# Optimization experiments

Hardware: AMD Instinct MI355X
Metric: run time of the kernel (lower is better)

The kernel has to match this reference:

```python
import jax, jax.numpy as jnp
import numpy as np

N_NODES = 200000
N_EDGES = 600000
IN_DIM = 130   # hidden_dim + 2
HID = 128
BN_EPS = 1e-5


def setup_inputs() -> dict:
    key = jax.random.key(0)
    ks = jax.random.split(key, 12)
    s = 0.05
    inp = {
        'x': jax.random.normal(ks[0], (N_NODES, IN_DIM), dtype=jnp.float32),
        'edge_index': jax.random.randint(ks[1], (2, N_EDGES), 0, N_NODES, dtype=jnp.int32),
        # SAGEConv 1: lin_l (aggregated neighbors, with bias), lin_r (root, no bias)
        'W1_l': jax.random.normal(ks[2], (IN_DIM, HID), dtype=jnp.float32) * s,
        'b1_l': jnp.zeros((HID,), dtype=jnp.float32),
        'W1_r': jax.random.normal(ks[3], (IN_DIM, HID), dtype=jnp.float32) * s,
        # BatchNorm1d(128) params + running stats (eval mode)
        'g1': jnp.ones((HID,), dtype=jnp.float32),
        'be1': jnp.zeros((HID,), dtype=jnp.float32),
        'rm1': jax.random.normal(ks[4], (HID,), dtype=jnp.float32) * 0.01,
        'rv1': jnp.ones((HID,), dtype=jnp.float32),
        # SAGEConv 2
        'W2_l': jax.random.normal(ks[5], (HID, HID), dtype=jnp.float32) * s,
        'b2_l': jnp.zeros((HID,), dtype=jnp.float32),
        'W2_r': jax.random.normal(ks[6], (HID, HID), dtype=jnp.float32) * s,
        'g2': jnp.ones((HID,), dtype=jnp.float32),
        'be2': jnp.zeros((HID,), dtype=jnp.float32),
        'rm2': jax.random.normal(ks[7], (HID,), dtype=jnp.float32) * 0.01,
        'rv2': jnp.ones((HID,), dtype=jnp.float32),
    }
    return inp


def _sage_mean(x, src, dst, W_l, b_l, W_r, n_nodes):
    # PyG SAGEConv (mean aggr): out = lin_l(mean_{j in N(i)} x_j) + lin_r(x_i)
    msg = x[src]                                                 # [E, F] gather
    agg = jax.ops.segment_sum(msg, dst, num_segments=n_nodes)    # [N, F]
    deg = jax.ops.segment_sum(jnp.ones((src.shape[0], 1), x.dtype), dst,
                              num_segments=n_nodes)              # [N, 1]
    mean = agg / jnp.maximum(deg, 1.0)
    return mean @ W_l + b_l + x @ W_r


def _bn_eval(x, g, b, rm, rv):
    return (x - rm) * (g * jax.lax.rsqrt(rv + BN_EPS)) + b


def reference(x, edge_index, W1_l, b1_l, W1_r, g1, be1, rm1, rv1,
              W2_l, b2_l, W2_r, g2, be2, rm2, rv2):
    src, dst = edge_index[0], edge_index[1]
    n = x.shape[0]
    h = _sage_mean(x, src, dst, W1_l, b1_l, W1_r, n)
    h = jax.nn.relu(_bn_eval(h, g1, be1, rm1, rv1))
    # dropout is identity in eval mode
    h = _sage_mean(h, src, dst, W2_l, b2_l, W2_r, n)
    h = jax.nn.relu(_bn_eval(h, g2, be2, rm2, rv2))
    return h
```

## Files before the change

kernel.cpp:

```cpp
#include <hip/hip_runtime.h>

typedef short v8s __attribute__((ext_vector_type(8)));
typedef float v4f __attribute__((ext_vector_type(4)));
typedef unsigned short v4us __attribute__((ext_vector_type(4)));

__device__ __forceinline__ unsigned short f2bf(float x) {
  union { float f; unsigned int u; } c; c.f = x;
  unsigned int u = c.u;
  return (unsigned short)((u + 0x7fffu + ((u >> 16) & 1u)) >> 16);
}
__device__ __forceinline__ float bf2f(unsigned int hi16) {
  union { unsigned int u; float f; } c; c.u = hi16 << 16;
  return c.f;
}
__device__ __forceinline__ ushort2 pk(float2 v) {
  ushort2 p; p.x = f2bf(v.x); p.y = f2bf(v.y); return p;
}

__global__ void bn_fold_k(const float* __restrict__ g1, const float* __restrict__ be1,
                          const float* __restrict__ rm1, const float* __restrict__ rv1,
                          const float* __restrict__ b1,
                          const float* __restrict__ g2, const float* __restrict__ be2,
                          const float* __restrict__ rm2, const float* __restrict__ rv2,
                          const float* __restrict__ b2,
                          float* __restrict__ s1, float* __restrict__ t1,
                          float* __restrict__ s2, float* __restrict__ t2,
                          unsigned short* __restrict__ bufA, int N) {
  int i = threadIdx.x;
  if (i < 128) {
    float sv = g1[i] * rsqrtf(rv1[i] + 1e-5f);
    s1[i] = sv; t1[i] = (b1[i] - rm1[i]) * sv + be1[i];
    float sw = g2[i] * rsqrtf(rv2[i] + 1e-5f);
    s2[i] = sw; t2[i] = (b2[i] - rm2[i]) * sw + be2[i];
  }
  if (i < 64) ((unsigned int*)(bufA + (long)N * 128))[i] = 0u;
}

template<int K, int KC>
__global__ void pack2_k(const float* __restrict__ Wl, const float* __restrict__ Wr,
                        unsigned short* __restrict__ wpk) {
  int i = blockIdx.x * 256 + threadIdx.x;
  if (i >= KC * 8192) return;
  int kk = i & 31, n = (i >> 5) & 255, kc = i >> 13;
  int k = kc * 32 + kk;
  float v = 0.f;
  if (k < K) v = (n < 128) ? Wl[k * 128 + n] : Wr[k * 128 + (n - 128)];
  wpk[i] = f2bf(v);
}

__global__ void zero_i_k(int* __restrict__ p, int n) {
  int i = blockIdx.x * 256 + threadIdx.x;
  if (i < n) p[i] = 0;
}
__global__ void count_k(const int* __restrict__ dst, int* __restrict__ degi, int E) {
  int i = blockIdx.x * 256 + threadIdx.x;
  if (i < E) atomicAdd(&degi[dst[i]], 1);
}
__global__ __launch_bounds__(256) void scan1_k(const int* __restrict__ degi,
                                               int* __restrict__ rowptr,
                                               int* __restrict__ bsum, int N) {
  __shared__ int sd[256];
  const int t = threadIdx.x;
  const int base = blockIdx.x * 1024 + t * 4;
  int v[4];
#pragma unroll
  for (int j = 0; j < 4; ++j) v[j] = (base + j < N) ? degi[base + j] : 0;
  const int tot = v[0] + v[1] + v[2] + v[3];
  sd[t] = tot;
  __syncthreads();
  for (int off = 1; off < 256; off <<= 1) {
    int o = (t >= off) ? sd[t - off] : 0;
    __syncthreads();
    sd[t] += o;
    __syncthreads();
  }
  int e = sd[t] - tot;
#pragma unroll
  for (int j = 0; j < 4; ++j) {
    if (base + j < N) rowptr[base + j] = e;
    e += v[j];
  }
  if (t == 255) bsum[blockIdx.x] = sd[255];
}
__global__ __launch_bounds__(256) void scan2_k(int* __restrict__ bsum, int nb) {
  __shared__ int sd[256];
  const int t = threadIdx.x;
  const int v = (t < nb) ? bsum[t] : 0;
  sd[t] = v;
  __syncthreads();
  for (int off = 1; off < 256; off <<= 1) {
    int o = (t >= off) ? sd[t - off] : 0;
    __syncthreads();
    sd[t] += o;
    __syncthreads();
  }
  if (t < nb) bsum[t] = sd[t] - v;
}
__global__ void scan3_k(int* __restrict__ rowptr, int* __restrict__ cursor,
                        const int* __restrict__ bsum, int N, int E) {
  int i = blockIdx.x * 256 + threadIdx.x;
  if (i < N) {
    int v = rowptr[i] + bsum[i >> 10];
    rowptr[i] = v;
    cursor[i] = v;
  } else if (i == N) {
    rowptr[N] = E;
  }
}
__global__ void fill_k(const int* __restrict__ src, const int* __restrict__ dst,
                       int* __restrict__ cursor, int* __restrict__ nbr, int E) {
  int i = blockIdx.x * 256 + threadIdx.x;
  if (i < E) {
    int p = atomicAdd(&cursor[dst[i]], 1);
    nbr[p] = src[i];
  }
}

template<int KC, bool SRCF32>
__global__ __launch_bounds__(256) void gemm2_k(const void* __restrict__ Asrc,
                                               const unsigned short* __restrict__ wpk,
                                               unsigned short* __restrict__ Ol,
                                               unsigned short* __restrict__ Or, int N) {
  constexpr int KP = KC * 32;
  constexpr int LDA = KP + 8;
  __shared__ __align__(16) unsigned short a_s[64][LDA];
  const int tid = threadIdx.x;
  const int node0 = blockIdx.x * 64;

  if constexpr (SRCF32) {
    {
      const int zr = tid >> 2, zq = tid & 3;
      v8s z = {0, 0, 0, 0, 0, 0, 0, 0};
      *(v8s*)&a_s[zr][136 + zq * 8] = z;
      if (tid < 192) {
        const int r3 = tid / 3, p3 = tid - 3 * r3;
        *(unsigned int*)&a_s[r3][130 + 2 * p3] = 0u;
      }
    }
    const float* xb = (const float*)Asrc + (long)node0 * 130;
    if (node0 + 64 <= N) {
      float4 v[9];
#pragma unroll
      for (int i = 0; i < 9; ++i) {
        const int g = i * 256 + tid;
        if (g < 2080) v[i] = *(const float4*)(xb + 4 * g);
      }
#pragma unroll
      for (int i = 0; i < 9; ++i) {
        const int g = i * 256 + tid;
        if (g < 2080) {
          const int p0 = 2 * g, p1 = 2 * g + 1;
          const int r0_ = (p0 * 4033) >> 18, r1_ = (p1 * 4033) >> 18;
          const int c0_ = p0 - 65 * r0_, c1_ = p1 - 65 * r1_;
          *(ushort2*)&a_s[r0_][2 * c0_] = pk(make_float2(v[i].x, v[i].y));
          *(ushort2*)&a_s[r1_][2 * c1_] = pk(make_float2(v[i].z, v[i].w));
        }
      }
    } else {
      for (int i = 0; i < 9; ++i) {
        const int g = i * 256 + tid;
        if (g < 2080) {
#pragma unroll
          for (int h = 0; h < 2; ++h) {
            const int p = 2 * g + h;
            const int r = (p * 4033) >> 18;
            const int c = p - 65 * r;
            float2 vv = make_float2(0.f, 0.f);
            if (node0 + r < N)
              vv = *(const float2*)((const float*)Asrc + (long)(node0 + r) * 130 + 2 * c);
            *(ushort2*)&a_s[r][2 * c] = pk(vv);
          }
        }
      }
    }
  } else {
    const unsigned short* hb = (const unsigned short*)Asrc + (long)node0 * 128;
    v8s v[KC];
#pragma unroll
    for (int i = 0; i < KC; ++i) {
      const int u = i * 256 + tid;
      const int r = u >> 4;
      v[i] = (v8s){0, 0, 0, 0, 0, 0, 0, 0};
      if (node0 + r < N) v[i] = *(const v8s*)(hb + 8 * u);
    }
#pragma unroll
    for (int i = 0; i < KC; ++i) {
      const int u = i * 256 + tid;
      *(v8s*)&a_s[u >> 4][(u & 15) * 8] = v[i];
    }
  }
  __syncthreads();

  const int wave = tid >> 6, lane = tid & 63;
  const int quad = lane >> 4, l16 = lane & 15;
  v4f acc[4][4];
#pragma unroll
  for (int mt = 0; mt < 4; ++mt)
#pragma unroll
    for (int nt = 0; nt < 4; ++nt) acc[mt][nt] = (v4f){0.f, 0.f, 0.f, 0.f};

  const unsigned short* wb = wpk + (wave * 64 + l16) * 32 + quad * 8;
#pragma unroll
  for (int kc = 0; kc < KC; ++kc) {
    v8s wf[4];
#pragma unroll
    for (int nt = 0; nt < 4; ++nt)
      wf[nt] = *(const v8s*)(wb + kc * 8192 + nt * 512);
#pragma unroll
    for (int mt = 0; mt < 4; ++mt) {
      v8s nf = *(const v8s*)(&a_s[mt * 16 + l16][kc * 32 + quad * 8]);
#pragma unroll
      for (int nt = 0; nt < 4; ++nt)
        acc[mt][nt] = __builtin_amdgcn_mfma_f32_16x16x32_bf16(wf[nt], nf, acc[mt][nt], 0, 0, 0);
    }
  }

  unsigned short* ob = (wave < 2) ? Ol : Or;
  const int cb = (wave & 1) * 64;
#pragma unroll
  for (int mt = 0; mt < 4; ++mt) {
    const int rw = node0 + mt * 16 + l16;
    if (rw < N) {
#pragma unroll
      for (int nt = 0; nt < 4; ++nt) {
        const int oc = cb + nt * 16 + quad * 4;
        v4us v;
        v[0] = f2bf(acc[mt][nt][0]);
        v[1] = f2bf(acc[mt][nt][1]);
        v[2] = f2bf(acc[mt][nt][2]);
        v[3] = f2bf(acc[mt][nt][3]);
        *(v4us*)(ob + (long)rw * 128 + oc) = v;
      }
    }
  }
}

template<bool OUTF32>
__global__ __launch_bounds__(256) void spmm_f_k(const unsigned short* __restrict__ gsrc,
                                                const unsigned short* __restrict__ rsrc,
                                                const int* __restrict__ rowptr,
                                                const int* __restrict__ nbr,
                                                const float* __restrict__ sc,
                                                const float* __restrict__ tc,
                                                void* __restrict__ out, int N) {
  const int w = threadIdx.x >> 6, lane = threadIdx.x & 63;
  const int nb = blockIdx.x * 16 + w * 4;
  if (nb >= N) return;

  int rp = 0;
  if (lane <= 4 && nb + lane <= N) rp = rowptr[nb + lane];
  int d[4], r0[4], myn[4];
  float2 a[4];
#pragma unroll
  for (int r = 0; r < 4; ++r) {
    r0[r] = __shfl(rp, r, 64);
    const int r1 = __shfl(rp, r + 1, 64);
    d[r] = (nb + r < N) ? (r1 - r0[r]) : 0;
    a[r] = make_float2(0.f, 0.f);
    myn[r] = N;
    if (lane < min(d[r], 64)) myn[r] = nbr[r0[r] + lane];
  }
  const int dm = max(max(d[0], d[1]), max(d[2], d[3]));

  if (dm <= 64) {
    for (int e0 = 0; e0 < dm; e0 += 8) {
      unsigned int u[4][8];
#pragma unroll
      for (int j = 0; j < 8; ++j)
#pragma unroll
        for (int r = 0; r < 4; ++r) {
          const int e = e0 + j;
          const int idx = (e < d[r]) ? __shfl(myn[r], e, 64) : N;
          u[r][j] = *(const unsigned int*)(gsrc + (long)idx * 128 + 2 * lane);
        }
#pragma unroll
      for (int r = 0; r < 4; ++r)
#pragma unroll
        for (int j = 0; j < 8; ++j) {
          a[r].x += bf2f(u[r][j] & 0xffffu);
          a[r].y += bf2f(u[r][j] >> 16);
        }
    }
  } else {
    for (int r = 0; r < 4; ++r) {
      for (int base = r0[r]; base < r0[r] + d[r]; base += 64) {
        const int cnt = min(64, r0[r] + d[r] - base);
        const int mn = (lane < cnt) ? nbr[base + lane] : N;
        for (int e = 0; e < cnt; ++e) {
          const unsigned int uu =
              *(const unsigned int*)(gsrc + (long)__shfl(mn, e, 64) * 128 + 2 * lane);
          a[r].x += bf2f(uu & 0xffffu);
          a[r].y += bf2f(uu >> 16);
        }
      }
    }
  }

  const float2 sv = *(const float2*)(sc + 2 * lane);
  const float2 tv = *(const float2*)(tc + 2 * lane);
#pragma unroll
  for (int r = 0; r < 4; ++r) {
    if (nb + r < N) {
      const float inv = 1.0f / fmaxf((float)d[r], 1.0f);
      const unsigned int ur = *(const unsigned int*)(rsrc + (long)(nb + r) * 128 + 2 * lane);
      float yx = a[r].x * inv + bf2f(ur & 0xffffu);
      float yy = a[r].y * inv + bf2f(ur >> 16);
      yx = fmaxf(yx * sv.x + tv.x, 0.f);
      yy = fmaxf(yy * sv.y + tv.y, 0.f);
      if (OUTF32) {
        *(float2*)((float*)out + (long)(nb + r) * 128 + 2 * lane) = make_float2(yx, yy);
      } else {
        *(ushort2*)((unsigned short*)out + (long)(nb + r) * 128 + 2 * lane) =
            pk(make_float2(yx, yy));
      }
    }
  }
}

extern "C" void kernel_launch(void* const* d_in, const int* in_sizes, int n_in,
                              void* d_out, int out_size, void* d_ws, size_t ws_size,
                              hipStream_t stream) {
  const float* x   = (const float*)d_in[0];
  const int*   ei  = (const int*)d_in[1];
  const float* W1l = (const float*)d_in[2];
  const float* b1  = (const float*)d_in[3];
  const float* W1r = (const float*)d_in[4];
  const float* g1  = (const float*)d_in[5];
  const float* be1 = (const float*)d_in[6];
  const float* rm1 = (const float*)d_in[7];
  const float* rv1 = (const float*)d_in[8];
  const float* W2l = (const float*)d_in[9];
  const float* b2  = (const float*)d_in[10];
  const float* W2r = (const float*)d_in[11];
  const float* g2  = (const float*)d_in[12];
  const float* be2 = (const float*)d_in[13];
  const float* rm2 = (const float*)d_in[14];
  const float* rv2 = (const float*)d_in[15];

  const int E = in_sizes[1] / 2;
  const int N = in_sizes[0] / 130;
  const int* src = ei;
  const int* dst = ei + E;

  unsigned short* bufA = (unsigned short*)d_ws;
  unsigned short* bufB = bufA + (size_t)(N + 1) * 128;
  unsigned short* wpka = bufB + (size_t)(N + 1) * 128;
  unsigned short* wpkb = wpka + 5 * 8192;
  float* s1 = (float*)(wpkb + 4 * 8192);
  float* t1 = s1 + 128;
  float* s2 = t1 + 128;
  float* t2 = s2 + 128;
  int* degi   = (int*)(t2 + 128);
  int* rowptr = degi + N;
  int* bsum   = rowptr + N + 1;
  int* nbr    = bsum + 256;

  hipLaunchKernelGGL(bn_fold_k, dim3(1), dim3(128), 0, stream,
                     g1, be1, rm1, rv1, b1, g2, be2, rm2, rv2, b2,
                     s1, t1, s2, t2, bufA, N);
  hipLaunchKernelGGL((pack2_k<130, 5>), dim3(160), dim3(256), 0, stream, W1l, W1r, wpka);
  hipLaunchKernelGGL((pack2_k<128, 4>), dim3(128), dim3(256), 0, stream, W2l, W2r, wpkb);

  hipLaunchKernelGGL(zero_i_k, dim3((N + 255) / 256), dim3(256), 0, stream, degi, N);
  hipLaunchKernelGGL(count_k, dim3((E + 255) / 256), dim3(256), 0, stream, dst, degi, E);
  const int nb = (N + 1023) / 1024;
  hipLaunchKernelGGL(scan1_k, dim3(nb), dim3(256), 0, stream, degi, rowptr, bsum, N);
  hipLaunchKernelGGL(scan2_k, dim3(1), dim3(256), 0, stream, bsum, nb);
  hipLaunchKernelGGL(scan3_k, dim3((N + 256) / 256), dim3(256), 0, stream,
                     rowptr, degi, bsum, N, E);
  hipLaunchKernelGGL(fill_k, dim3((E + 255) / 256), dim3(256), 0, stream,
                     src, dst, degi, nbr, E);

  const int ngb = (N + 63) / 64;
  const int nsb = (N + 15) / 16;

  hipLaunchKernelGGL((gemm2_k<5, true>), dim3(ngb), dim3(256), 0, stream,
                     (const void*)x, wpka, bufA, bufB, N);
  hipLaunchKernelGGL((spmm_f_k<false>), dim3(nsb), dim3(256), 0, stream,
                     bufA, bufB, rowptr, nbr, s1, t1, (void*)bufB, N);
  hipLaunchKernelGGL((gemm2_k<4, false>), dim3(ngb), dim3(256), 0, stream,
                     (const void*)bufB, wpkb, bufA, bufB, N);
  hipLaunchKernelGGL((spmm_f_k<true>), dim3(nsb), dim3(256), 0, stream,
                     bufA, bufB, rowptr, nbr, s2, t2, d_out, N);
}
```

Baseline: 447.2 us.

## Fuse root-term GEMM into neighbor-aggregation kernel instead of materializing it

The two-output GEMM that produced both the neighbor-projected and root-projected features is split. The GEMM kernel now computes only the neighbor (lin_l) projection. The root (lin_r) projection is computed inside the aggregation kernel with MFMA on a 16-node tile staged in LDS, so the root output is never written to or read back from global memory. The trade-off is that layer 1 reads the fp32 input x a second time, and the gather kernel gains extra LDS, MFMA work and barriers, which may hurt its latency hiding.

```diff
diff --git a/kernel.cpp b/kernel.cpp
--- a/kernel.cpp
+++ b/kernel.cpp
@@ -37,15 +37,12 @@
 }
 
 template<int K, int KC>
-__global__ void pack2_k(const float* __restrict__ Wl, const float* __restrict__ Wr,
-                        unsigned short* __restrict__ wpk) {
+__global__ void pack1_k(const float* __restrict__ W, unsigned short* __restrict__ wpk) {
   int i = blockIdx.x * 256 + threadIdx.x;
-  if (i >= KC * 8192) return;
-  int kk = i & 31, n = (i >> 5) & 255, kc = i >> 13;
+  if (i >= KC * 4096) return;
+  int kk = i & 31, n = (i >> 5) & 127, kc = i >> 12;
   int k = kc * 32 + kk;
-  float v = 0.f;
-  if (k < K) v = (n < 128) ? Wl[k * 128 + n] : Wr[k * 128 + (n - 128)];
-  wpk[i] = f2bf(v);
+  wpk[i] = (k < K) ? f2bf(W[k * 128 + n]) : (unsigned short)0;
 }
 
 __global__ void zero_i_k(int* __restrict__ p, int n) {
@@ -117,10 +114,9 @@
 }
 
 template<int KC, bool SRCF32>
-__global__ __launch_bounds__(256) void gemm2_k(const void* __restrict__ Asrc,
+__global__ __launch_bounds__(256) void gemmL_k(const void* __restrict__ Asrc,
                                                const unsigned short* __restrict__ wpk,
-                                               unsigned short* __restrict__ Ol,
-                                               unsigned short* __restrict__ Or, int N) {
+                                               unsigned short* __restrict__ O, int N) {
   constexpr int KP = KC * 32;
   constexpr int LDA = KP + 8;
   __shared__ __align__(16) unsigned short a_s[64][LDA];
@@ -193,60 +189,119 @@
 
   const int wave = tid >> 6, lane = tid & 63;
   const int quad = lane >> 4, l16 = lane & 15;
-  v4f acc[4][4];
+  v4f acc[4][2];
 #pragma unroll
   for (int mt = 0; mt < 4; ++mt)
 #pragma unroll
-    for (int nt = 0; nt < 4; ++nt) acc[mt][nt] = (v4f){0.f, 0.f, 0.f, 0.f};
-
-  const unsigned short* wb = wpk + (wave * 64 + l16) * 32 + quad * 8;
+    for (int nt = 0; nt < 2; ++nt) acc[mt][nt] = (v4f){0.f, 0.f, 0.f, 0.f};
+
+  const unsigned short* wb = wpk + (wave * 32 + l16) * 32 + quad * 8;
 #pragma unroll
   for (int kc = 0; kc < KC; ++kc) {
-    v8s wf[4];
-#pragma unroll
-    for (int nt = 0; nt < 4; ++nt)
-      wf[nt] = *(const v8s*)(wb + kc * 8192 + nt * 512);
+    v8s wf[2];
+#pragma unroll
+    for (int nt = 0; nt < 2; ++nt)
+      wf[nt] = *(const v8s*)(wb + kc * 4096 + nt * 512);
 #pragma unroll
     for (int mt = 0; mt < 4; ++mt) {
       v8s nf = *(const v8s*)(&a_s[mt * 16 + l16][kc * 32 + quad * 8]);
 #pragma unroll
-      for (int nt = 0; nt < 4; ++nt)
+      for (int nt = 0; nt < 2; ++nt)
         acc[mt][nt] = __builtin_amdgcn_mfma_f32_16x16x32_bf16(wf[nt], nf, acc[mt][nt], 0, 0, 0);
     }
   }
 
-  unsigned short* ob = (wave < 2) ? Ol : Or;
-  const int cb = (wave & 1) * 64;
 #pragma unroll
   for (int mt = 0; mt < 4; ++mt) {
     const int rw = node0 + mt * 16 + l16;
     if (rw < N) {
 #pragma unroll
-      for (int nt = 0; nt < 4; ++nt) {
-        const int oc = cb + nt * 16 + quad * 4;
+      for (int nt = 0; nt < 2; ++nt) {
+        const int oc = wave * 32 + nt * 16 + quad * 4;
         v4us v;
         v[0] = f2bf(acc[mt][nt][0]);
         v[1] = f2bf(acc[mt][nt][1]);
         v[2] = f2bf(acc[mt][nt][2]);
         v[3] = f2bf(acc[mt][nt][3]);
-        *(v4us*)(ob + (long)rw * 128 + oc) = v;
-      }
-    }
-  }
-}
-
-template<bool OUTF32>
-__global__ __launch_bounds__(256) void spmm_f_k(const unsigned short* __restrict__ gsrc,
-                                                const unsigned short* __restrict__ rsrc,
-                                                const int* __restrict__ rowptr,
-                                                const int* __restrict__ nbr,
-                                                const float* __restrict__ sc,
-                                                const float* __restrict__ tc,
-                                                void* __restrict__ out, int N) {
-  const int w = threadIdx.x >> 6, lane = threadIdx.x & 63;
-  const int nb = blockIdx.x * 16 + w * 4;
-  if (nb >= N) return;
-
+        *(v4us*)(O + (long)rw * 128 + oc) = v;
+      }
+    }
+  }
+}
+
+template<int KC, bool SRCF32, bool OUTF32>
+__global__ __launch_bounds__(256) void spmmR_k(const unsigned short* __restrict__ gsrc,
+                                               const void* __restrict__ rsrc,
+                                               const unsigned short* __restrict__ wpkr,
+                                               const int* __restrict__ rowptr,
+                                               const int* __restrict__ nbr,
+                                               const float* __restrict__ sc,
+                                               const float* __restrict__ tc,
+                                               void* __restrict__ out, int N) {
+  constexpr int LXS = SRCF32 ? 168 : 136;
+  __shared__ __align__(16) unsigned short xls[16][LXS];
+  __shared__ __align__(16) float rls[16][132];
+  const int tid = threadIdx.x;
+  const int w = tid >> 6, lane = tid & 63;
+  const int quad = lane >> 4, l16 = lane & 15;
+  const int nb0 = blockIdx.x * 16;
+
+  if constexpr (SRCF32) {
+    {
+      if (tid < 64) {
+        v8s z = {0, 0, 0, 0, 0, 0, 0, 0};
+        *(v8s*)&xls[tid >> 2][136 + (tid & 3) * 8] = z;
+      }
+      if (tid < 48) {
+        const int r3 = tid / 3, p3 = tid - 3 * r3;
+        *(unsigned int*)&xls[r3][130 + 2 * p3] = 0u;
+      }
+    }
+    const float* xb = (const float*)rsrc + (long)nb0 * 130;
+    if (nb0 + 16 <= N) {
+      float4 v[3];
+#pragma unroll
+      for (int i = 0; i < 3; ++i) {
+        const int g = i * 256 + tid;
+        if (g < 520) v[i] = *(const float4*)(xb + 4 * g);
+      }
+#pragma unroll
+      for (int i = 0; i < 3; ++i) {
+        const int g = i * 256 + tid;
+        if (g < 520) {
+          const int p0 = 2 * g, p1 = 2 * g + 1;
+          const int r0_ = (p0 * 4033) >> 18, r1_ = (p1 * 4033) >> 18;
+          const int c0_ = p0 - 65 * r0_, c1_ = p1 - 65 * r1_;
+          *(ushort2*)&xls[r0_][2 * c0_] = pk(make_float2(v[i].x, v[i].y));
+          *(ushort2*)&xls[r1_][2 * c1_] = pk(make_float2(v[i].z, v[i].w));
+        }
+      }
+    } else {
+      for (int i = 0; i < 3; ++i) {
+        const int g = i * 256 + tid;
+        if (g < 520) {
+#pragma unroll
+          for (int h = 0; h < 2; ++h) {
+            const int p = 2 * g + h;
+            const int r = (p * 4033) >> 18;
+            const int c = p - 65 * r;
+            float2 vv = make_float2(0.f, 0.f);
+            if (nb0 + r < N)
+              vv = *(const float2*)((const float*)rsrc + (long)(nb0 + r) * 130 + 2 * c);
+            *(ushort2*)&xls[r][2 * c] = pk(vv);
+          }
+        }
+      }
+    }
+  } else {
+    const unsigned short* hb = (const unsigned short*)rsrc + (long)nb0 * 128;
+    const int r = tid >> 4, c = (tid & 15) * 8;
+    v8s v = {0, 0, 0, 0, 0, 0, 0, 0};
+    if (nb0 + r < N) v = *(const v8s*)(hb + (long)r * 128 + c);
+    *(v8s*)&xls[r][c] = v;
+  }
+
+  const int nb = nb0 + w * 4;
   int rp = 0;
   if (lane <= 4 && nb + lane <= N) rp = rowptr[nb + lane];
   int d[4], r0[4], myn[4];
@@ -261,6 +316,27 @@
     if (lane < min(d[r], 64)) myn[r] = nbr[r0[r] + lane];
   }
   const int dm = max(max(d[0], d[1]), max(d[2], d[3]));
+
+  __syncthreads();
+
+  {
+    v4f racc[2];
+    racc[0] = (v4f){0.f, 0.f, 0.f, 0.f};
+    racc[1] = (v4f){0.f, 0.f, 0.f, 0.f};
+    const unsigned short* wb = wpkr + (w * 32 + l16) * 32 + quad * 8;
+#pragma unroll
+    for (int kc = 0; kc < KC; ++kc) {
+      v8s nf = *(const v8s*)&xls[l16][kc * 32 + quad * 8];
+#pragma unroll
+      for (int nt = 0; nt < 2; ++nt) {
+        v8s wf = *(const v8s*)(wb + kc * 4096 + nt * 512);
+        racc[nt] = __builtin_amdgcn_mfma_f32_16x16x32_bf16(wf, nf, racc[nt], 0, 0, 0);
+      }
+    }
+#pragma unroll
+    for (int nt = 0; nt < 2; ++nt)
+      *(v4f*)&rls[l16][w * 32 + nt * 16 + quad * 4] = racc[nt];
+  }
 
   if (dm <= 64) {
     for (int e0 = 0; e0 < dm; e0 += 8) {
@@ -296,15 +372,17 @@
     }
   }
 
+  __syncthreads();
+
   const float2 sv = *(const float2*)(sc + 2 * lane);
   const float2 tv = *(const float2*)(tc + 2 * lane);
 #pragma unroll
   for (int r = 0; r < 4; ++r) {
     if (nb + r < N) {
       const float inv = 1.0f / fmaxf((float)d[r], 1.0f);
-      const unsigned int ur = *(const unsigned int*)(rsrc + (long)(nb + r) * 128 + 2 * lane);
-      float yx = a[r].x * inv + bf2f(ur & 0xffffu);
-      float yy = a[r].y * inv + bf2f(ur >> 16);
+      const float2 rt = *(const float2*)&rls[w * 4 + r][2 * lane];
+      float yx = a[r].x * inv + rt.x;
+      float yy = a[r].y * inv + rt.y;
       yx = fmaxf(yx * sv.x + tv.x, 0.f);
       yy = fmaxf(yy * sv.y + tv.y, 0.f);
       if (OUTF32) {
@@ -344,9 +422,11 @@
 
   unsigned short* bufA = (unsigned short*)d_ws;
   unsigned short* bufB = bufA + (size_t)(N + 1) * 128;
-  unsigned short* wpka = bufB + (size_t)(N + 1) * 128;
-  unsigned short* wpkb = wpka + 5 * 8192;
-  float* s1 = (float*)(wpkb + 4 * 8192);
+  unsigned short* wp1l = bufB + (size_t)(N + 1) * 128;
+  unsigned short* wp1r = wp1l + 5 * 4096;
+  unsigned short* wp2l = wp1r + 5 * 4096;
+  unsigned short* wp2r = wp2l + 4 * 4096;
+  float* s1 = (float*)(wp2r + 4 * 4096);
   float* t1 = s1 + 128;
   float* s2 = t1 + 128;
   float* t2 = s2 + 128;
@@ -358,8 +438,10 @@
   hipLaunchKernelGGL(bn_fold_k, dim3(1), dim3(128), 0, stream,
                      g1, be1, rm1, rv1, b1, g2, be2, rm2, rv2, b2,
                      s1, t1, s2, t2, bufA, N);
-  hipLaunchKernelGGL((pack2_k<130, 5>), dim3(160), dim3(256), 0, stream, W1l, W1r, wpka);
-  hipLaunchKernelGGL((pack2_k<128, 4>), dim3(128), dim3(256), 0, stream, W2l, W2r, wpkb);
+  hipLaunchKernelGGL((pack1_k<130, 5>), dim3(80), dim3(256), 0, stream, W1l, wp1l);
+  hipLaunchKernelGGL((pack1_k<130, 5>), dim3(80), dim3(256), 0, stream, W1r, wp1r);
+  hipLaunchKernelGGL((pack1_k<128, 4>), dim3(64), dim3(256), 0, stream, W2l, wp2l);
+  hipLaunchKernelGGL((pack1_k<128, 4>), dim3(64), dim3(256), 0, stream, W2r, wp2r);
 
   hipLaunchKernelGGL(zero_i_k, dim3((N + 255) / 256), dim3(256), 0, stream, degi, N);
   hipLaunchKernelGGL(count_k, dim3((E + 255) / 256), dim3(256), 0, stream, dst, degi, E);
@@ -374,12 +456,12 @@
   const int ngb = (N + 63) / 64;
   const int nsb = (N + 15) / 16;
 
-  hipLaunchKernelGGL((gemm2_k<5, true>), dim3(ngb), dim3(256), 0, stream,
-                     (const void*)x, wpka, bufA, bufB, N);
-  hipLaunchKernelGGL((spmm_f_k<false>), dim3(nsb), dim3(256), 0, stream,
-                     bufA, bufB, rowptr, nbr, s1, t1, (void*)bufB, N);
-  hipLaunchKernelGGL((gemm2_k<4, false>), dim3(ngb), dim3(256), 0, stream,
-                     (const void*)bufB, wpkb, bufA, bufB, N);
-  hipLaunchKernelGGL((spmm_f_k<true>), dim3(nsb), dim3(256), 0, stream,
-                     bufA, bufB, rowptr, nbr, s2, t2, d_out, N);
-}
+  hipLaunchKernelGGL((gemmL_k<5, true>), dim3(ngb), dim3(256), 0, stream,
+                     (const void*)x, wp1l, bufA, N);
+  hipLaunchKernelGGL((spmmR_k<5, true, false>), dim3(nsb), dim3(256), 0, stream,
+                     bufA, (const void*)x, wp1r, rowptr, nbr, s1, t1, (void*)bufB, N);
+  hipLaunchKernelGGL((gemmL_k<4, false>), dim3(ngb), dim3(256), 0, stream,
+                     (const void*)bufB, wp2l, bufA, N);
+  hipLaunchKernelGGL((spmmR_k<4, false, true>), dim3(nsb), dim3(256), 0, stream,
+                     bufA, (const void*)bufB, wp2r, rowptr, nbr, s2, t2, d_out, N);
+}
```

Measured after the change: 460.8 us. 3.1% more time.
